# Optimization experiments

Hardware: AMD Instinct MI355X
Metric: run time of the kernel (lower is better)

Reference implementation:

```python
import jax, jax.numpy as jnp
import numpy as np

N_NODES = 50000
N_EDGES = 800000
IN_CH = 128
HID = 64
OUT_CH = 64


def sage_conv(x, src, dst, w_l, w_r, b, num_nodes):
    """PyG SAGEConv with mean aggregation: lin_l(mean_j x_j) + lin_r(x_i)."""
    # gather source features and scatter-mean into destination nodes
    agg = jax.ops.segment_sum(x[src], dst, num_segments=num_nodes)          # [N, C]
    deg = jax.ops.segment_sum(jnp.ones((src.shape[0],), x.dtype), dst,
                              num_segments=num_nodes)                        # [N]
    mean = agg / jnp.maximum(deg, 1.0)[:, None]
    return mean @ w_l + x @ w_r + b


def setup_inputs() -> dict:
    key = jax.random.key(0)
    k = jax.random.split(key, 8)
    x = jax.random.normal(k[0], (N_NODES, IN_CH), dtype=jnp.float32)
    edge_index = jax.random.randint(k[1], (2, N_EDGES), 0, N_NODES, dtype=jnp.int32)
    s1 = 1.0 / np.sqrt(IN_CH)
    s2 = 1.0 / np.sqrt(HID)
    w1_l = jax.random.uniform(k[2], (IN_CH, HID), jnp.float32, -s1, s1)
    w1_r = jax.random.uniform(k[3], (IN_CH, HID), jnp.float32, -s1, s1)
    b1 = jax.random.uniform(k[4], (HID,), jnp.float32, -s1, s1)
    w2_l = jax.random.uniform(k[5], (HID, OUT_CH), jnp.float32, -s2, s2)
    w2_r = jax.random.uniform(k[6], (HID, OUT_CH), jnp.float32, -s2, s2)
    b2 = jax.random.uniform(k[7], (OUT_CH,), jnp.float32, -s2, s2)
    return {"x": x, "edge_index": edge_index,
            "w1_l": w1_l, "w1_r": w1_r, "b1": b1,
            "w2_l": w2_l, "w2_r": w2_r, "b2": b2}


def reference(x, edge_index, w1_l, w1_r, b1, w2_l, w2_r, b2):
    src, dst = edge_index[0], edge_index[1]
    num_nodes = x.shape[0]
    h = jax.nn.relu(sage_conv(x, src, dst, w1_l, w1_r, b1, num_nodes))
    out = jax.nn.relu(sage_conv(h, src, dst, w2_l, w2_r, b2, num_nodes))
    return out
```

## Files before the change

kernel.cpp:

```cpp
#include <hip/hip_runtime.h>
#include <hip/hip_fp16.h>

#define DEGCAP 64
#define NB_MAX 256
#define BCAP 5120
#define TILE 4000

typedef _Float16 half8 __attribute__((ext_vector_type(8)));
typedef float float4v __attribute__((ext_vector_type(4)));

__global__ __launch_bounds__(256) void prep(int* __restrict__ bCursor,
                                            const float* __restrict__ w1l,
                                            const float* __restrict__ w1r,
                                            const float* __restrict__ w2l,
                                            const float* __restrict__ w2r,
                                            _Float16* __restrict__ Wt1,
                                            _Float16* __restrict__ Wt2) {
    const int gtid = blockIdx.x * 256 + threadIdx.x;
    const int gstride = gridDim.x * 256;
    if (gtid < NB_MAX) bCursor[gtid] = 0;
    for (int i = gtid; i < 128 * 128; i += gstride) {
        int c = i >> 7, k = i & 127;
        const float* W = (c < 64) ? w1l : w1r;
        Wt1[c * 128 + k] = (_Float16)W[k * 64 + (c & 63)];
    }
    for (int i = gtid; i < 128 * 64; i += gstride) {
        int c = i >> 6, k = i & 63;
        const float* W = (c < 64) ? w2l : w2r;
        Wt2[c * 64 + k] = (_Float16)W[k * 64 + (c & 63)];
    }
}

template <int K, bool AF32>
__device__ __forceinline__ void gemm_body(const void* __restrict__ Av,
                                          const _Float16* __restrict__ Wt,
                                          unsigned short* __restrict__ Clh,
                                          unsigned short* __restrict__ Trh,
                                          int M, int blk) {
    constexpr int NS = K / 32;
    const int tid = threadIdx.x;
    const int row0 = blk * 64;
    const int wv = tid >> 6;
    const int lane = tid & 63;
    const int qd = lane >> 4;
    const int lr = lane & 15;
    const int col = wv * 16 + lr;

    half8 bl[NS], br[NS];
    #pragma unroll
    for (int s = 0; s < NS; ++s) {
        bl[s] = *(const half8*)&Wt[col * K + s * 32 + qd * 8];
        br[s] = *(const half8*)&Wt[(64 + col) * K + s * 32 + qd * 8];
    }

    half8 a[4][NS];
    #pragma unroll
    for (int i = 0; i < 4; ++i) {
        const int gr = row0 + i * 16 + lr;
        const bool ok = gr < M;
        if constexpr (AF32) {
            const float* Arow = (const float*)Av + (long long)gr * K;
            #pragma unroll
            for (int s = 0; s < NS; ++s) {
                float4 t0 = make_float4(0.f, 0.f, 0.f, 0.f);
                float4 t1 = make_float4(0.f, 0.f, 0.f, 0.f);
                if (ok) {
                    t0 = *(const float4*)&Arow[s * 32 + qd * 8];
                    t1 = *(const float4*)&Arow[s * 32 + qd * 8 + 4];
                }
                half8 h;
                h[0] = (_Float16)t0.x; h[1] = (_Float16)t0.y;
                h[2] = (_Float16)t0.z; h[3] = (_Float16)t0.w;
                h[4] = (_Float16)t1.x; h[5] = (_Float16)t1.y;
                h[6] = (_Float16)t1.z; h[7] = (_Float16)t1.w;
                a[i][s] = h;
            }
        } else {
            const _Float16* Arow = (const _Float16*)Av + (long long)gr * K;
            #pragma unroll
            for (int s = 0; s < NS; ++s) {
                a[i][s] = ok ? *(const half8*)&Arow[s * 32 + qd * 8]
                             : (half8){0, 0, 0, 0, 0, 0, 0, 0};
            }
        }
    }

    float4v accL[4], accR[4];
    #pragma unroll
    for (int i = 0; i < 4; ++i) {
        accL[i] = (float4v){0.f, 0.f, 0.f, 0.f};
        accR[i] = (float4v){0.f, 0.f, 0.f, 0.f};
    }

    #pragma unroll
    for (int i = 0; i < 4; ++i) {
        #pragma unroll
        for (int s = 0; s < NS; ++s) {
            accL[i] = __builtin_amdgcn_mfma_f32_16x16x32_f16(a[i][s], bl[s], accL[i], 0, 0, 0);
            accR[i] = __builtin_amdgcn_mfma_f32_16x16x32_f16(a[i][s], br[s], accR[i], 0, 0, 0);
        }
    }

    #pragma unroll
    for (int i = 0; i < 4; ++i) {
        #pragma unroll
        for (int rg = 0; rg < 4; ++rg) {
            int gr = row0 + i * 16 + qd * 4 + rg;
            if (gr < M) {
                Clh[(long long)gr * 64 + col] = __half_as_ushort(__float2half_rn(accL[i][rg]));
                Trh[(long long)gr * 64 + col] = __half_as_ushort(__float2half_rn(accR[i][rg]));
            }
        }
    }
}

__global__ __launch_bounds__(256) void fused_scatter_gemm1(
        const int* __restrict__ src, const int* __restrict__ dst,
        int* __restrict__ bCursor, unsigned int* __restrict__ gPacked,
        int E, int NB, int scatterBlocks,
        const float* __restrict__ A, const _Float16* __restrict__ Wt1,
        unsigned short* __restrict__ Clh, unsigned short* __restrict__ Trh,
        int M) {
    __shared__ __align__(16) char smem[22048];
    const int tid = threadIdx.x;

    if ((int)blockIdx.x < scatterBlocks) {
        unsigned int* spv = (unsigned int*)smem;
        unsigned char* sbuk = (unsigned char*)(smem + 16000);
        int* hist = (int*)(smem + 20000);
        int* cur  = (int*)(smem + 21024);

        const int t0 = blockIdx.x * TILE;
        const int len = (E - t0) < TILE ? (E - t0) : TILE;

        hist[tid] = 0;
        __syncthreads();
        for (int j = tid; j < len; j += 256) {
            int d = dst[t0 + j];
            int s = src[t0 + j];
            int b = d >> 8;
            sbuk[j] = (unsigned char)b;
            spv[j] = ((unsigned int)(d & 255) << 17) | (unsigned int)s;
            atomicAdd(&hist[b], 1);
        }
        __syncthreads();
        if (tid < NB && hist[tid] > 0)
            cur[tid] = tid * BCAP + atomicAdd(&bCursor[tid], hist[tid]);
        __syncthreads();
        for (int j = tid; j < len; j += 256) {
            int b = sbuk[j];
            int pos = atomicAdd(&cur[b], 1);
            if (pos < (b + 1) * BCAP) gPacked[pos] = spv[j];
        }
    } else {
        gemm_body<128, true>(A, Wt1, Clh, Trh, M, (int)blockIdx.x - scatterBlocks);
    }
}

__global__ __launch_bounds__(256) void bucket_build(const unsigned int* __restrict__ gPacked,
                                                    const int* __restrict__ bCursor,
                                                    int* __restrict__ deg,
                                                    unsigned short* __restrict__ ssrc,
                                                    int N) {
    __shared__ int cnt[256];
    const int tid = threadIdx.x;
    const int b = blockIdx.x;
    const int base = b * BCAP;
    int C = bCursor[b];
    if (C > BCAP) C = BCAP;

    cnt[tid] = 0;
    __syncthreads();
    for (int j = tid; j < C; j += 256) {
        unsigned int v = gPacked[base + j];
        int ln = v >> 17;
        int pos = atomicAdd(&cnt[ln], 1);
        if (pos < DEGCAP)
            ssrc[(long long)(b * 256 + ln) * DEGCAP + pos] = (unsigned short)(v & 0x1FFFFu);
    }
    __syncthreads();
    int node = b * 256 + tid;
    if (node < N) deg[node] = cnt[tid] < DEGCAP ? cnt[tid] : DEGCAP;
}

__global__ __launch_bounds__(256) void gemm2(const _Float16* __restrict__ Ah,
                                             const _Float16* __restrict__ Wt2,
                                             unsigned short* __restrict__ Clh,
                                             unsigned short* __restrict__ Trh,
                                             int M) {
    gemm_body<64, false>(Ah, Wt2, Clh, Trh, M, (int)blockIdx.x);
}

template <bool OUTH>
__global__ __launch_bounds__(256) void agg_combine(const unsigned int* __restrict__ tl2,
                                                   const unsigned int* __restrict__ trh2,
                                                   const float* __restrict__ bias,
                                                   const int* __restrict__ deg_,
                                                   const unsigned short* __restrict__ ssrc,
                                                   void* __restrict__ outv, int N) {
    int w = (blockIdx.x * 256 + threadIdx.x) >> 6;
    int lane = threadIdx.x & 63;
    if (w >= N) return;
    int deg = deg_[w];
    int n = deg < DEGCAP ? deg : DEGCAP;
    int g2 = lane >> 4;
    int c8 = lane & 15;

    int sid = (lane < n) ? (int)ssrc[(long long)w * DEGCAP + lane] : 0;

    float ax0 = 0.f, ay0 = 0.f, ax1 = 0.f, ay1 = 0.f;

    #pragma unroll 2
    for (int jj = 0; jj < n; jj += 8) {
        int e0 = __shfl(sid, jj + g2, 64);
        int e1 = __shfl(sid, jj + 4 + g2, 64);
        bool v0 = (jj + g2) < n;
        bool v1 = (jj + 4 + g2) < n;
        uint2 u0 = make_uint2(0u, 0u), u1 = make_uint2(0u, 0u);
        if (v0) u0 = *(const uint2*)&tl2[(long long)e0 * 32 + c8 * 2];
        if (v1) u1 = *(const uint2*)&tl2[(long long)e1 * 32 + c8 * 2];
        float2 f;
        f = __half22float2(*(__half2*)&u0.x); ax0 += f.x; ay0 += f.y;
        f = __half22float2(*(__half2*)&u0.y); ax1 += f.x; ay1 += f.y;
        f = __half22float2(*(__half2*)&u1.x); ax0 += f.x; ay0 += f.y;
        f = __half22float2(*(__half2*)&u1.y); ax1 += f.x; ay1 += f.y;
    }

    ax0 += __shfl_xor(ax0, 16, 64);
    ay0 += __shfl_xor(ay0, 16, 64);
    ax1 += __shfl_xor(ax1, 16, 64);
    ay1 += __shfl_xor(ay1, 16, 64);
    ax0 += __shfl_xor(ax0, 32, 64);
    ay0 += __shfl_xor(ay0, 32, 64);
    ax1 += __shfl_xor(ax1, 32, 64);
    ay1 += __shfl_xor(ay1, 32, 64);

    if (g2 == 0) {
        float d = (float)(deg > 1 ? deg : 1);
        uint2 tu = *(const uint2*)&trh2[(long long)w * 32 + c8 * 2];
        float2 t0 = __half22float2(*(__half2*)&tu.x);
        float2 t1 = __half22float2(*(__half2*)&tu.y);
        float4 bb = *(const float4*)&bias[c8 * 4];
        float v0 = fmaxf(ax0 / d + t0.x + bb.x, 0.f);
        float v1 = fmaxf(ay0 / d + t0.y + bb.y, 0.f);
        float v2 = fmaxf(ax1 / d + t1.x + bb.z, 0.f);
        float v3 = fmaxf(ay1 / d + t1.y + bb.w, 0.f);
        if (OUTH) {
            __half2 h0 = __floats2half2_rn(v0, v1);
            __half2 h1 = __floats2half2_rn(v2, v3);
            uint2 st;
            st.x = *(unsigned int*)&h0;
            st.y = *(unsigned int*)&h1;
            ((uint2*)outv)[(long long)w * 16 + c8] = st;
        } else {
            ((float4*)outv)[(long long)w * 16 + c8] = make_float4(v0, v1, v2, v3);
        }
    }
}

extern "C" void kernel_launch(void* const* d_in, const int* in_sizes, int n_in,
                              void* d_out, int out_size, void* d_ws, size_t ws_size,
                              hipStream_t stream) {
    const float* x   = (const float*)d_in[0];
    const int*   ei  = (const int*)d_in[1];
    const float* w1l = (const float*)d_in[2];
    const float* w1r = (const float*)d_in[3];
    const float* b1  = (const float*)d_in[4];
    const float* w2l = (const float*)d_in[5];
    const float* w2r = (const float*)d_in[6];
    const float* b2  = (const float*)d_in[7];
    float* out = (float*)d_out;

    const int N = in_sizes[0] / 128;
    const int E = in_sizes[1] / 2;
    const int* src = ei;
    const int* dst = ei + E;
    const int NB = (N + 255) >> 8;

    auto alignup = [](size_t v) { return (v + 255) & ~(size_t)255; };
    char* p = (char*)d_ws;
    int* bCursor = (int*)p;                    p += alignup(NB_MAX * sizeof(int));
    int* deg     = (int*)p;                    p += alignup((size_t)N * sizeof(int));
    unsigned int* gPacked = (unsigned int*)p;  p += alignup((size_t)NB_MAX * BCAP * sizeof(unsigned int));
    unsigned short* ssrc = (unsigned short*)p; p += alignup((size_t)N * DEGCAP * sizeof(unsigned short));
    const long long NC = (long long)N * 64;
    unsigned short* tlh = (unsigned short*)p;  p += alignup((size_t)NC * sizeof(unsigned short));
    unsigned short* trh = (unsigned short*)p;  p += alignup((size_t)NC * sizeof(unsigned short));
    unsigned short* hh  = (unsigned short*)p;  p += alignup((size_t)NC * sizeof(unsigned short));
    _Float16* Wt1 = (_Float16*)p;              p += alignup(128 * 128 * sizeof(_Float16));
    _Float16* Wt2 = (_Float16*)p;              p += alignup(128 * 64 * sizeof(_Float16));

    const int scatterBlocks = (E + TILE - 1) / TILE;
    const int gemmBlocks = (N + 63) / 64;
    const int aggBlocks = (int)((NC + 255) / 256);

    prep<<<96, 256, 0, stream>>>(bCursor, w1l, w1r, w2l, w2r, Wt1, Wt2);

    fused_scatter_gemm1<<<scatterBlocks + gemmBlocks, 256, 0, stream>>>(
        src, dst, bCursor, gPacked, E, NB, scatterBlocks,
        x, Wt1, tlh, trh, N);

    bucket_build<<<NB, 256, 0, stream>>>(gPacked, bCursor, deg, ssrc, N);

    agg_combine<true><<<aggBlocks, 256, 0, stream>>>((const unsigned int*)tlh,
                                                     (const unsigned int*)trh,
                                                     b1, deg, ssrc, hh, N);

    gemm2<<<gemmBlocks, 256, 0, stream>>>((const _Float16*)hh, Wt2, tlh, trh, N);
    agg_combine<false><<<aggBlocks, 256, 0, stream>>>((const unsigned int*)tlh,
                                                      (const unsigned int*)trh,
                                                      b2, deg, ssrc, out, N);
}
```

Baseline: 179.9 us.

## Split neighbor aggregation into two column-half passes to shrink gather working set

Each aggregation kernel is split into two launches, each covering half of the 64 feature columns (32 fp16 values, 64 bytes per row). A wave now gathers 8 neighbors per iteration at 8 bytes per lane, and the partial sums need an extra cross-lane reduction step. The aim is to halve the gathered table footprint per pass so random neighbor reads hit cache more often. The cost is reading the index lists twice, doubling launches, and adding shuffle work.

```diff
diff --git a/kernel.cpp b/kernel.cpp
--- a/kernel.cpp
+++ b/kernel.cpp
@@ -191,20 +191,20 @@
     gemm_body<64, false>(Ah, Wt2, Clh, Trh, M, (int)blockIdx.x);
 }
 
-template <bool OUTH>
-__global__ __launch_bounds__(256) void agg_combine(const unsigned int* __restrict__ tl2,
-                                                   const unsigned int* __restrict__ trh2,
-                                                   const float* __restrict__ bias,
-                                                   const int* __restrict__ deg_,
-                                                   const unsigned short* __restrict__ ssrc,
-                                                   void* __restrict__ outv, int N) {
+template <bool OUTH, int PASS>
+__global__ __launch_bounds__(256) void agg_half(const unsigned int* __restrict__ tl2,
+                                                const unsigned int* __restrict__ trh2,
+                                                const float* __restrict__ bias,
+                                                const int* __restrict__ deg_,
+                                                const unsigned short* __restrict__ ssrc,
+                                                void* __restrict__ outv, int N) {
     int w = (blockIdx.x * 256 + threadIdx.x) >> 6;
     int lane = threadIdx.x & 63;
     if (w >= N) return;
     int deg = deg_[w];
     int n = deg < DEGCAP ? deg : DEGCAP;
-    int g2 = lane >> 4;
-    int c8 = lane & 15;
+    int g8 = lane >> 3;
+    int c4 = lane & 7;
 
     int sid = (lane < n) ? (int)ssrc[(long long)w * DEGCAP + lane] : 0;
 
@@ -212,20 +212,19 @@
 
     #pragma unroll 2
     for (int jj = 0; jj < n; jj += 8) {
-        int e0 = __shfl(sid, jj + g2, 64);
-        int e1 = __shfl(sid, jj + 4 + g2, 64);
-        bool v0 = (jj + g2) < n;
-        bool v1 = (jj + 4 + g2) < n;
-        uint2 u0 = make_uint2(0u, 0u), u1 = make_uint2(0u, 0u);
-        if (v0) u0 = *(const uint2*)&tl2[(long long)e0 * 32 + c8 * 2];
-        if (v1) u1 = *(const uint2*)&tl2[(long long)e1 * 32 + c8 * 2];
+        int e = __shfl(sid, jj + g8, 64);
+        bool v = (jj + g8) < n;
+        uint2 u = make_uint2(0u, 0u);
+        if (v) u = *(const uint2*)&tl2[(long long)e * 32 + PASS * 16 + c4 * 2];
         float2 f;
-        f = __half22float2(*(__half2*)&u0.x); ax0 += f.x; ay0 += f.y;
-        f = __half22float2(*(__half2*)&u0.y); ax1 += f.x; ay1 += f.y;
-        f = __half22float2(*(__half2*)&u1.x); ax0 += f.x; ay0 += f.y;
-        f = __half22float2(*(__half2*)&u1.y); ax1 += f.x; ay1 += f.y;
-    }
-
+        f = __half22float2(*(__half2*)&u.x); ax0 += f.x; ay0 += f.y;
+        f = __half22float2(*(__half2*)&u.y); ax1 += f.x; ay1 += f.y;
+    }
+
+    ax0 += __shfl_xor(ax0, 8, 64);
+    ay0 += __shfl_xor(ay0, 8, 64);
+    ax1 += __shfl_xor(ax1, 8, 64);
+    ay1 += __shfl_xor(ay1, 8, 64);
     ax0 += __shfl_xor(ax0, 16, 64);
     ay0 += __shfl_xor(ay0, 16, 64);
     ax1 += __shfl_xor(ax1, 16, 64);
@@ -235,12 +234,12 @@
     ax1 += __shfl_xor(ax1, 32, 64);
     ay1 += __shfl_xor(ay1, 32, 64);
 
-    if (g2 == 0) {
+    if (g8 == 0) {
         float d = (float)(deg > 1 ? deg : 1);
-        uint2 tu = *(const uint2*)&trh2[(long long)w * 32 + c8 * 2];
+        uint2 tu = *(const uint2*)&trh2[(long long)w * 32 + PASS * 16 + c4 * 2];
         float2 t0 = __half22float2(*(__half2*)&tu.x);
         float2 t1 = __half22float2(*(__half2*)&tu.y);
-        float4 bb = *(const float4*)&bias[c8 * 4];
+        float4 bb = *(const float4*)&bias[PASS * 32 + c4 * 4];
         float v0 = fmaxf(ax0 / d + t0.x + bb.x, 0.f);
         float v1 = fmaxf(ay0 / d + t0.y + bb.y, 0.f);
         float v2 = fmaxf(ax1 / d + t1.x + bb.z, 0.f);
@@ -251,9 +250,10 @@
             uint2 st;
             st.x = *(unsigned int*)&h0;
             st.y = *(unsigned int*)&h1;
-            ((uint2*)outv)[(long long)w * 16 + c8] = st;
+            ((uint2*)outv)[(long long)w * 16 + PASS * 8 + c4] = st;
         } else {
-            ((float4*)outv)[(long long)w * 16 + c8] = make_float4(v0, v1, v2, v3);
+            ((float4*)outv)[(long long)w * 16 + PASS * 8 + c4] =
+                make_float4(v0, v1, v2, v3);
         }
     }
 }
@@ -302,12 +302,19 @@
 
     bucket_build<<<NB, 256, 0, stream>>>(gPacked, bCursor, deg, ssrc, N);
 
-    agg_combine<true><<<aggBlocks, 256, 0, stream>>>((const unsigned int*)tlh,
+    agg_half<true, 0><<<aggBlocks, 256, 0, stream>>>((const unsigned int*)tlh,
                                                      (const unsigned int*)trh,
                                                      b1, deg, ssrc, hh, N);
+    agg_half<true, 1><<<aggBlocks, 256, 0, stream>>>((const unsigned int*)tlh,
+                                                     (const unsigned int*)trh,
+                                                     b1, deg, ssrc, hh, N);
 
     gemm2<<<gemmBlocks, 256, 0, stream>>>((const _Float16*)hh, Wt2, tlh, trh, N);
-    agg_combine<false><<<aggBlocks, 256, 0, stream>>>((const unsigned int*)tlh,
+
+    agg_half<false, 0><<<aggBlocks, 256, 0, stream>>>((const unsigned int*)tlh,
                                                       (const unsigned int*)trh,
                                                       b2, deg, ssrc, out, N);
-}
+    agg_half<false, 1><<<aggBlocks, 256, 0, stream>>>((const unsigned int*)tlh,
+                                                      (const unsigned int*)trh,
+                                                      b2, deg, ssrc, out, N);
+}
```

Measured after the change: 216.8 us. 1.21x slower.

## Split lin_l output into two column-half arrays and aggregate each half separately

Applied to the files above, without the earlier changes.

The GEMMs now write the neighbour-transformed features into two separate 32-column fp16 arrays instead of one 64-column array. Aggregation runs as two passes in one doubled grid, each gathering only one half, so each pass's gather working set is half the size and may fit better in cache. The cost is twice as many waves, with degree, source-index and shuffle overhead repeated per pass. Each gathered load also shrinks from 8 to 4 bytes per lane.

```diff
diff --git a/kernel.cpp b/kernel.cpp
--- a/kernel.cpp
+++ b/kernel.cpp
@@ -34,7 +34,8 @@
 template <int K, bool AF32>
 __device__ __forceinline__ void gemm_body(const void* __restrict__ Av,
                                           const _Float16* __restrict__ Wt,
-                                          unsigned short* __restrict__ Clh,
+                                          unsigned short* __restrict__ Cl_lo,
+                                          unsigned short* __restrict__ Cl_hi,
                                           unsigned short* __restrict__ Trh,
                                           int M, int blk) {
     constexpr int NS = K / 32;
@@ -101,13 +102,15 @@
         }
     }
 
+    unsigned short* ClT = (wv < 2) ? Cl_lo : Cl_hi;
+    const int colh = col & 31;
     #pragma unroll
     for (int i = 0; i < 4; ++i) {
         #pragma unroll
         for (int rg = 0; rg < 4; ++rg) {
             int gr = row0 + i * 16 + qd * 4 + rg;
             if (gr < M) {
-                Clh[(long long)gr * 64 + col] = __half_as_ushort(__float2half_rn(accL[i][rg]));
+                ClT[(long long)gr * 32 + colh] = __half_as_ushort(__float2half_rn(accL[i][rg]));
                 Trh[(long long)gr * 64 + col] = __half_as_ushort(__float2half_rn(accR[i][rg]));
             }
         }
@@ -119,8 +122,8 @@
         int* __restrict__ bCursor, unsigned int* __restrict__ gPacked,
         int E, int NB, int scatterBlocks,
         const float* __restrict__ A, const _Float16* __restrict__ Wt1,
-        unsigned short* __restrict__ Clh, unsigned short* __restrict__ Trh,
-        int M) {
+        unsigned short* __restrict__ Cl_lo, unsigned short* __restrict__ Cl_hi,
+        unsigned short* __restrict__ Trh, int M) {
     __shared__ __align__(16) char smem[22048];
     const int tid = threadIdx.x;
 
@@ -153,7 +156,8 @@
             if (pos < (b + 1) * BCAP) gPacked[pos] = spv[j];
         }
     } else {
-        gemm_body<128, true>(A, Wt1, Clh, Trh, M, (int)blockIdx.x - scatterBlocks);
+        gemm_body<128, true>(A, Wt1, Cl_lo, Cl_hi, Trh, M,
+                             (int)blockIdx.x - scatterBlocks);
     }
 }
 
@@ -185,75 +189,78 @@
 
 __global__ __launch_bounds__(256) void gemm2(const _Float16* __restrict__ Ah,
                                              const _Float16* __restrict__ Wt2,
-                                             unsigned short* __restrict__ Clh,
+                                             unsigned short* __restrict__ Cl_lo,
+                                             unsigned short* __restrict__ Cl_hi,
                                              unsigned short* __restrict__ Trh,
                                              int M) {
-    gemm_body<64, false>(Ah, Wt2, Clh, Trh, M, (int)blockIdx.x);
+    gemm_body<64, false>(Ah, Wt2, Cl_lo, Cl_hi, Trh, M, (int)blockIdx.x);
 }
 
 template <bool OUTH>
-__global__ __launch_bounds__(256) void agg_combine(const unsigned int* __restrict__ tl2,
-                                                   const unsigned int* __restrict__ trh2,
-                                                   const float* __restrict__ bias,
-                                                   const int* __restrict__ deg_,
-                                                   const unsigned short* __restrict__ ssrc,
-                                                   void* __restrict__ outv, int N) {
-    int w = (blockIdx.x * 256 + threadIdx.x) >> 6;
+__global__ __launch_bounds__(256) void agg_split(const unsigned int* __restrict__ tl_lo,
+                                                 const unsigned int* __restrict__ tl_hi,
+                                                 const unsigned int* __restrict__ trh2,
+                                                 const float* __restrict__ bias,
+                                                 const int* __restrict__ deg_,
+                                                 const unsigned short* __restrict__ ssrc,
+                                                 void* __restrict__ outv,
+                                                 int N, int aggBlocks) {
+    const int pass = ((int)blockIdx.x >= aggBlocks) ? 1 : 0;
+    const int vb = (int)blockIdx.x - pass * aggBlocks;
+    int w = (vb * 256 + threadIdx.x) >> 6;
     int lane = threadIdx.x & 63;
     if (w >= N) return;
+    const unsigned int* tl = pass ? tl_hi : tl_lo;
     int deg = deg_[w];
     int n = deg < DEGCAP ? deg : DEGCAP;
-    int g2 = lane >> 4;
-    int c8 = lane & 15;
+    int g4 = lane >> 4;
+    int c2 = lane & 15;
 
     int sid = (lane < n) ? (int)ssrc[(long long)w * DEGCAP + lane] : 0;
 
-    float ax0 = 0.f, ay0 = 0.f, ax1 = 0.f, ay1 = 0.f;
-
-    #pragma unroll 2
-    for (int jj = 0; jj < n; jj += 8) {
-        int e0 = __shfl(sid, jj + g2, 64);
-        int e1 = __shfl(sid, jj + 4 + g2, 64);
-        bool v0 = (jj + g2) < n;
-        bool v1 = (jj + 4 + g2) < n;
-        uint2 u0 = make_uint2(0u, 0u), u1 = make_uint2(0u, 0u);
-        if (v0) u0 = *(const uint2*)&tl2[(long long)e0 * 32 + c8 * 2];
-        if (v1) u1 = *(const uint2*)&tl2[(long long)e1 * 32 + c8 * 2];
+    float x0 = 0.f, y0 = 0.f, x1 = 0.f, y1 = 0.f;
+    float x2 = 0.f, y2 = 0.f, x3 = 0.f, y3 = 0.f;
+
+    for (int jj = 0; jj < n; jj += 16) {
+        int e0 = __shfl(sid, jj + g4, 64);
+        int e1 = __shfl(sid, jj + 4 + g4, 64);
+        int e2 = __shfl(sid, jj + 8 + g4, 64);
+        int e3 = __shfl(sid, jj + 12 + g4, 64);
+        bool v0 = (jj + g4) < n;
+        bool v1 = (jj + 4 + g4) < n;
+        bool v2 = (jj + 8 + g4) < n;
+        bool v3 = (jj + 12 + g4) < n;
+        unsigned int u0 = 0u, u1 = 0u, u2 = 0u, u3 = 0u;
+        if (v0) u0 = tl[e0 * 16 + c2];
+        if (v1) u1 = tl[e1 * 16 + c2];
+        if (v2) u2 = tl[e2 * 16 + c2];
+        if (v3) u3 = tl[e3 * 16 + c2];
         float2 f;
-        f = __half22float2(*(__half2*)&u0.x); ax0 += f.x; ay0 += f.y;
-        f = __half22float2(*(__half2*)&u0.y); ax1 += f.x; ay1 += f.y;
-        f = __half22float2(*(__half2*)&u1.x); ax0 += f.x; ay0 += f.y;
-        f = __half22float2(*(__half2*)&u1.y); ax1 += f.x; ay1 += f.y;
-    }
-
-    ax0 += __shfl_xor(ax0, 16, 64);
-    ay0 += __shfl_xor(ay0, 16, 64);
-    ax1 += __shfl_xor(ax1, 16, 64);
-    ay1 += __shfl_xor(ay1, 16, 64);
-    ax0 += __shfl_xor(ax0, 32, 64);
-    ay0 += __shfl_xor(ay0, 32, 64);
-    ax1 += __shfl_xor(ax1, 32, 64);
-    ay1 += __shfl_xor(ay1, 32, 64);
-
-    if (g2 == 0) {
+        f = __half22float2(*(__half2*)&u0); x0 += f.x; y0 += f.y;
+        f = __half22float2(*(__half2*)&u1); x1 += f.x; y1 += f.y;
+        f = __half22float2(*(__half2*)&u2); x2 += f.x; y2 += f.y;
+        f = __half22float2(*(__half2*)&u3); x3 += f.x; y3 += f.y;
+    }
+
+    float sx = (x0 + x1) + (x2 + x3);
+    float sy = (y0 + y1) + (y2 + y3);
+    sx += __shfl_xor(sx, 16, 64);
+    sy += __shfl_xor(sy, 16, 64);
+    sx += __shfl_xor(sx, 32, 64);
+    sy += __shfl_xor(sy, 32, 64);
+
+    if (g4 == 0) {
         float d = (float)(deg > 1 ? deg : 1);
-        uint2 tu = *(const uint2*)&trh2[(long long)w * 32 + c8 * 2];
-        float2 t0 = __half22float2(*(__half2*)&tu.x);
-        float2 t1 = __half22float2(*(__half2*)&tu.y);
-        float4 bb = *(const float4*)&bias[c8 * 4];
-        float v0 = fmaxf(ax0 / d + t0.x + bb.x, 0.f);
-        float v1 = fmaxf(ay0 / d + t0.y + bb.y, 0.f);
-        float v2 = fmaxf(ax1 / d + t1.x + bb.z, 0.f);
-        float v3 = fmaxf(ay1 / d + t1.y + bb.w, 0.f);
+        unsigned int tu = trh2[(long long)w * 32 + pass * 16 + c2];
+        float2 t = __half22float2(*(__half2*)&tu);
+        float2 bb = *(const float2*)&bias[pass * 32 + c2 * 2];
+        float v0 = fmaxf(sx / d + t.x + bb.x, 0.f);
+        float v1 = fmaxf(sy / d + t.y + bb.y, 0.f);
         if (OUTH) {
-            __half2 h0 = __floats2half2_rn(v0, v1);
-            __half2 h1 = __floats2half2_rn(v2, v3);
-            uint2 st;
-            st.x = *(unsigned int*)&h0;
-            st.y = *(unsigned int*)&h1;
-            ((uint2*)outv)[(long long)w * 16 + c8] = st;
+            __half2 hv = __floats2half2_rn(v0, v1);
+            ((unsigned int*)outv)[(long long)w * 32 + pass * 16 + c2] = *(unsigned int*)&hv;
         } else {
-            ((float4*)outv)[(long long)w * 16 + c8] = make_float4(v0, v1, v2, v3);
+            ((float2*)outv)[(long long)w * 32 + pass * 16 + c2] = make_float2(v0, v1);
         }
     }
 }
@@ -284,30 +291,35 @@
     unsigned int* gPacked = (unsigned int*)p;  p += alignup((size_t)NB_MAX * BCAP * sizeof(unsigned int));
     unsigned short* ssrc = (unsigned short*)p; p += alignup((size_t)N * DEGCAP * sizeof(unsigned short));
     const long long NC = (long long)N * 64;
-    unsigned short* tlh = (unsigned short*)p;  p += alignup((size_t)NC * sizeof(unsigned short));
-    unsigned short* trh = (unsigned short*)p;  p += alignup((size_t)NC * sizeof(unsigned short));
-    unsigned short* hh  = (unsigned short*)p;  p += alignup((size_t)NC * sizeof(unsigned short));
-    _Float16* Wt1 = (_Float16*)p;              p += alignup(128 * 128 * sizeof(_Float16));
-    _Float16* Wt2 = (_Float16*)p;              p += alignup(128 * 64 * sizeof(_Float16));
+    unsigned short* tl_lo = (unsigned short*)p; p += alignup((size_t)N * 32 * sizeof(unsigned short));
+    unsigned short* tl_hi = (unsigned short*)p; p += alignup((size_t)N * 32 * sizeof(unsigned short));
+    unsigned short* trh = (unsigned short*)p;   p += alignup((size_t)NC * sizeof(unsigned short));
+    unsigned short* hh  = (unsigned short*)p;   p += alignup((size_t)NC * sizeof(unsigned short));
+    _Float16* Wt1 = (_Float16*)p;               p += alignup(128 * 128 * sizeof(_Float16));
+    _Float16* Wt2 = (_Float16*)p;               p += alignup(128 * 64 * sizeof(_Float16));
 
     const int scatterBlocks = (E + TILE - 1) / TILE;
     const int gemmBlocks = (N + 63) / 64;
     const int aggBlocks = (int)((NC + 255) / 256);
+    const int aggGrid = aggBlocks * 2;
 
     prep<<<96, 256, 0, stream>>>(bCursor, w1l, w1r, w2l, w2r, Wt1, Wt2);
 
     fused_scatter_gemm1<<<scatterBlocks + gemmBlocks, 256, 0, stream>>>(
         src, dst, bCursor, gPacked, E, NB, scatterBlocks,
-        x, Wt1, tlh, trh, N);
+        x, Wt1, tl_lo, tl_hi, trh, N);
 
     bucket_build<<<NB, 256, 0, stream>>>(gPacked, bCursor, deg, ssrc, N);
 
-    agg_combine<true><<<aggBlocks, 256, 0, stream>>>((const unsigned int*)tlh,
-                                                     (const unsigned int*)trh,
-                                                     b1, deg, ssrc, hh, N);
-
-    gemm2<<<gemmBlocks, 256, 0, stream>>>((const _Float16*)hh, Wt2, tlh, trh, N);
-    agg_combine<false><<<aggBlocks, 256, 0, stream>>>((const unsigned int*)tlh,
-                                                      (const unsigned int*)trh,
-                                                      b2, deg, ssrc, out, N);
-}
+    agg_split<true><<<aggGrid, 256, 0, stream>>>((const unsigned int*)tl_lo,
+                                                 (const unsigned int*)tl_hi,
+                                                 (const unsigned int*)trh,
+                                                 b1, deg, ssrc, hh, N, aggBlocks);
+
+    gemm2<<<gemmBlocks, 256, 0, stream>>>((const _Float16*)hh, Wt2,
+                                          tl_lo, tl_hi, trh, N);
+    agg_split<false><<<aggGrid, 256, 0, stream>>>((const unsigned int*)tl_lo,
+                                                  (const unsigned int*)tl_hi,
+                                                  (const unsigned int*)trh,
+                                                  b2, deg, ssrc, out, N, aggBlocks);
+}
```

After: 198.6 us. 1.1x slower.

## Store transformed neighbor features in column slices for cache-local aggregation

Applied to the files above, without the earlier changes.

The GEMM now writes the left-projected features in four 16-column slices, each stored contiguously across all nodes, instead of row-major 64-wide rows. The aggregation kernel assigns each block to one slice, so concurrently running blocks gather from a 1.6 MB slice that fits better in L2/MALL rather than the full feature table. This trades wider 16-byte gathers for 4-byte gathers and quadruples the number of index loads and degree reads per node.

```diff
diff --git a/kernel.cpp b/kernel.cpp
--- a/kernel.cpp
+++ b/kernel.cpp
@@ -5,6 +5,7 @@
 #define NB_MAX 256
 #define BCAP 5120
 #define TILE 4000
+#define NSLICE 4
 
 typedef _Float16 half8 __attribute__((ext_vector_type(8)));
 typedef float float4v __attribute__((ext_vector_type(4)));
@@ -34,7 +35,7 @@
 template <int K, bool AF32>
 __device__ __forceinline__ void gemm_body(const void* __restrict__ Av,
                                           const _Float16* __restrict__ Wt,
-                                          unsigned short* __restrict__ Clh,
+                                          unsigned short* __restrict__ Cls,
                                           unsigned short* __restrict__ Trh,
                                           int M, int blk) {
     constexpr int NS = K / 32;
@@ -107,8 +108,9 @@
         for (int rg = 0; rg < 4; ++rg) {
             int gr = row0 + i * 16 + qd * 4 + rg;
             if (gr < M) {
-                Clh[(long long)gr * 64 + col] = __half_as_ushort(__float2half_rn(accL[i][rg]));
-                Trh[(long long)gr * 64 + col] = __half_as_ushort(__float2half_rn(accR[i][rg]));
+                Cls[((size_t)wv * M + gr) * 16 + lr] =
+                    __half_as_ushort(__float2half_rn(accL[i][rg]));
+                Trh[(size_t)gr * 64 + col] = __half_as_ushort(__float2half_rn(accR[i][rg]));
             }
         }
     }
@@ -119,7 +121,7 @@
         int* __restrict__ bCursor, unsigned int* __restrict__ gPacked,
         int E, int NB, int scatterBlocks,
         const float* __restrict__ A, const _Float16* __restrict__ Wt1,
-        unsigned short* __restrict__ Clh, unsigned short* __restrict__ Trh,
+        unsigned short* __restrict__ Cls, unsigned short* __restrict__ Trh,
         int M) {
     __shared__ __align__(16) char smem[22048];
     const int tid = threadIdx.x;
@@ -153,7 +155,7 @@
             if (pos < (b + 1) * BCAP) gPacked[pos] = spv[j];
         }
     } else {
-        gemm_body<128, true>(A, Wt1, Clh, Trh, M, (int)blockIdx.x - scatterBlocks);
+        gemm_body<128, true>(A, Wt1, Cls, Trh, M, (int)blockIdx.x - scatterBlocks);
     }
 }
 
@@ -185,75 +187,65 @@
 
 __global__ __launch_bounds__(256) void gemm2(const _Float16* __restrict__ Ah,
                                              const _Float16* __restrict__ Wt2,
-                                             unsigned short* __restrict__ Clh,
+                                             unsigned short* __restrict__ Cls,
                                              unsigned short* __restrict__ Trh,
                                              int M) {
-    gemm_body<64, false>(Ah, Wt2, Clh, Trh, M, (int)blockIdx.x);
+    gemm_body<64, false>(Ah, Wt2, Cls, Trh, M, (int)blockIdx.x);
 }
 
 template <bool OUTH>
-__global__ __launch_bounds__(256) void agg_combine(const unsigned int* __restrict__ tl2,
-                                                   const unsigned int* __restrict__ trh2,
-                                                   const float* __restrict__ bias,
-                                                   const int* __restrict__ deg_,
-                                                   const unsigned short* __restrict__ ssrc,
-                                                   void* __restrict__ outv, int N) {
-    int w = (blockIdx.x * 256 + threadIdx.x) >> 6;
-    int lane = threadIdx.x & 63;
+__global__ __launch_bounds__(256) void agg_slice(
+        const unsigned int* __restrict__ tls,
+        const unsigned int* __restrict__ trh2,
+        const float* __restrict__ bias,
+        const int* __restrict__ deg_,
+        const unsigned short* __restrict__ ssrc,
+        void* __restrict__ outv, int N) {
+    const int s = (int)blockIdx.x & 3;
+    const int vb = (int)blockIdx.x >> 2;
+    const int wv = threadIdx.x >> 6;
+    const int lane = threadIdx.x & 63;
+    const int w = vb * 4 + wv;
     if (w >= N) return;
-    int deg = deg_[w];
-    int n = deg < DEGCAP ? deg : DEGCAP;
-    int g2 = lane >> 4;
-    int c8 = lane & 15;
-
-    int sid = (lane < n) ? (int)ssrc[(long long)w * DEGCAP + lane] : 0;
-
-    float ax0 = 0.f, ay0 = 0.f, ax1 = 0.f, ay1 = 0.f;
-
-    #pragma unroll 2
-    for (int jj = 0; jj < n; jj += 8) {
-        int e0 = __shfl(sid, jj + g2, 64);
-        int e1 = __shfl(sid, jj + 4 + g2, 64);
-        bool v0 = (jj + g2) < n;
-        bool v1 = (jj + 4 + g2) < n;
-        uint2 u0 = make_uint2(0u, 0u), u1 = make_uint2(0u, 0u);
-        if (v0) u0 = *(const uint2*)&tl2[(long long)e0 * 32 + c8 * 2];
-        if (v1) u1 = *(const uint2*)&tl2[(long long)e1 * 32 + c8 * 2];
-        float2 f;
-        f = __half22float2(*(__half2*)&u0.x); ax0 += f.x; ay0 += f.y;
-        f = __half22float2(*(__half2*)&u0.y); ax1 += f.x; ay1 += f.y;
-        f = __half22float2(*(__half2*)&u1.x); ax0 += f.x; ay0 += f.y;
-        f = __half22float2(*(__half2*)&u1.y); ax1 += f.x; ay1 += f.y;
-    }
-
-    ax0 += __shfl_xor(ax0, 16, 64);
-    ay0 += __shfl_xor(ay0, 16, 64);
-    ax1 += __shfl_xor(ax1, 16, 64);
-    ay1 += __shfl_xor(ay1, 16, 64);
-    ax0 += __shfl_xor(ax0, 32, 64);
-    ay0 += __shfl_xor(ay0, 32, 64);
-    ax1 += __shfl_xor(ax1, 32, 64);
-    ay1 += __shfl_xor(ay1, 32, 64);
-
-    if (g2 == 0) {
+
+    const int deg = deg_[w];
+    const int n = deg < DEGCAP ? deg : DEGCAP;
+    const int eg = lane >> 3;
+    const int c = lane & 7;
+
+    int sid = (lane < n) ? (int)ssrc[(size_t)w * DEGCAP + lane] : 0;
+    const unsigned int* base = tls + (size_t)s * N * 8;
+
+    float ax = 0.f, ay = 0.f, bx = 0.f, by = 0.f;
+    for (int jj = 0; jj < n; jj += 16) {
+        int e0 = __shfl(sid, jj + eg, 64);
+        int e1 = __shfl(sid, jj + 8 + eg, 64);
+        bool v0 = (jj + eg) < n;
+        bool v1 = (jj + 8 + eg) < n;
+        unsigned int u0 = 0u, u1 = 0u;
+        if (v0) u0 = base[(size_t)e0 * 8 + c];
+        if (v1) u1 = base[(size_t)e1 * 8 + c];
+        float2 f0 = __half22float2(*(__half2*)&u0);
+        float2 f1 = __half22float2(*(__half2*)&u1);
+        ax += f0.x; ay += f0.y;  bx += f1.x; by += f1.y;
+    }
+    ax += bx; ay += by;
+    ax += __shfl_xor(ax, 8, 64);  ay += __shfl_xor(ay, 8, 64);
+    ax += __shfl_xor(ax, 16, 64); ay += __shfl_xor(ay, 16, 64);
+    ax += __shfl_xor(ax, 32, 64); ay += __shfl_xor(ay, 32, 64);
+
+    if (eg == 0) {
         float d = (float)(deg > 1 ? deg : 1);
-        uint2 tu = *(const uint2*)&trh2[(long long)w * 32 + c8 * 2];
-        float2 t0 = __half22float2(*(__half2*)&tu.x);
-        float2 t1 = __half22float2(*(__half2*)&tu.y);
-        float4 bb = *(const float4*)&bias[c8 * 4];
-        float v0 = fmaxf(ax0 / d + t0.x + bb.x, 0.f);
-        float v1 = fmaxf(ay0 / d + t0.y + bb.y, 0.f);
-        float v2 = fmaxf(ax1 / d + t1.x + bb.z, 0.f);
-        float v3 = fmaxf(ay1 / d + t1.y + bb.w, 0.f);
+        unsigned int tu = trh2[(size_t)w * 32 + s * 8 + c];
+        float2 t = __half22float2(*(__half2*)&tu);
+        float2 bb = *(const float2*)&bias[s * 16 + c * 2];
+        float v0 = fmaxf(ax / d + t.x + bb.x, 0.f);
+        float v1 = fmaxf(ay / d + t.y + bb.y, 0.f);
         if (OUTH) {
-            __half2 h0 = __floats2half2_rn(v0, v1);
-            __half2 h1 = __floats2half2_rn(v2, v3);
-            uint2 st;
-            st.x = *(unsigned int*)&h0;
-            st.y = *(unsigned int*)&h1;
-            ((uint2*)outv)[(long long)w * 16 + c8] = st;
+            __half2 hv = __floats2half2_rn(v0, v1);
+            ((unsigned int*)outv)[(size_t)w * 32 + s * 8 + c] = *(unsigned int*)&hv;
         } else {
-            ((float4*)outv)[(long long)w * 16 + c8] = make_float4(v0, v1, v2, v3);
+            ((float2*)outv)[(size_t)w * 32 + s * 8 + c] = make_float2(v0, v1);
         }
     }
 }
@@ -284,7 +276,7 @@
     unsigned int* gPacked = (unsigned int*)p;  p += alignup((size_t)NB_MAX * BCAP * sizeof(unsigned int));
     unsigned short* ssrc = (unsigned short*)p; p += alignup((size_t)N * DEGCAP * sizeof(unsigned short));
     const long long NC = (long long)N * 64;
-    unsigned short* tlh = (unsigned short*)p;  p += alignup((size_t)NC * sizeof(unsigned short));
+    unsigned short* tls = (unsigned short*)p;  p += alignup((size_t)NC * sizeof(unsigned short));
     unsigned short* trh = (unsigned short*)p;  p += alignup((size_t)NC * sizeof(unsigned short));
     unsigned short* hh  = (unsigned short*)p;  p += alignup((size_t)NC * sizeof(unsigned short));
     _Float16* Wt1 = (_Float16*)p;              p += alignup(128 * 128 * sizeof(_Float16));
@@ -292,22 +284,23 @@
 
     const int scatterBlocks = (E + TILE - 1) / TILE;
     const int gemmBlocks = (N + 63) / 64;
-    const int aggBlocks = (int)((NC + 255) / 256);
+    const int aggGrid = ((N + 3) / 4) * NSLICE;
 
     prep<<<96, 256, 0, stream>>>(bCursor, w1l, w1r, w2l, w2r, Wt1, Wt2);
 
     fused_scatter_gemm1<<<scatterBlocks + gemmBlocks, 256, 0, stream>>>(
         src, dst, bCursor, gPacked, E, NB, scatterBlocks,
-        x, Wt1, tlh, trh, N);
+        x, Wt1, tls, trh, N);
 
     bucket_build<<<NB, 256, 0, stream>>>(gPacked, bCursor, deg, ssrc, N);
 
-    agg_combine<true><<<aggBlocks, 256, 0, stream>>>((const unsigned int*)tlh,
-                                                     (const unsigned int*)trh,
-                                                     b1, deg, ssrc, hh, N);
-
-    gemm2<<<gemmBlocks, 256, 0, stream>>>((const _Float16*)hh, Wt2, tlh, trh, N);
-    agg_combine<false><<<aggBlocks, 256, 0, stream>>>((const unsigned int*)tlh,
-                                                      (const unsigned int*)trh,
-                                                      b2, deg, ssrc, out, N);
-}
+    agg_slice<true><<<aggGrid, 256, 0, stream>>>((const unsigned int*)tls,
+                                                 (const unsigned int*)trh,
+                                                 b1, deg, ssrc, hh, N);
+
+    gemm2<<<gemmBlocks, 256, 0, stream>>>((const _Float16*)hh, Wt2,
+                                          tls, trh, N);
+    agg_slice<false><<<aggGrid, 256, 0, stream>>>((const unsigned int*)tls,
+                                                  (const unsigned int*)trh,
+                                                  b2, deg, ssrc, out, N);
+}
```

Measured after the change: 244.9 us. 1.36x slower.
